# Performance work log

Hardware: AMD Instinct MI355X
Metric: run time of the kernel (lower is better)

## Reference

```python
import jax, jax.numpy as jnp
import numpy as np

M, N = 1024, 4096


def setup_inputs() -> dict:
    key = jax.random.key(0)
    k1, k2, k3 = jax.random.split(key, 3)
    scores = jax.random.normal(k1, (M, N), dtype=jnp.float32)
    continuing_ag = jax.random.randint(k2, (M,), 0, 2).astype(jnp.int32)
    joint_action_prev = jax.random.randint(k3, (M,), 0, N).astype(jnp.int32)
    return {"scores": scores, "continuing_ag": continuing_ag,
            "joint_action_prev": joint_action_prev}


def _assign(policy, continuing_ag, joint_action_prev):
    """Sequential greedy bipartite assignment (train=False / argmax path)."""
    m, n = policy.shape
    cont = continuing_ag.astype(bool)
    # Pre-assign continuing agents and zero their rows and chosen columns.
    out0 = jnp.where(cont, joint_action_prev, jnp.full((m,), -1, jnp.int32))
    col_hit = (jnp.zeros((n,), jnp.float32)
               .at[joint_action_prev].add(continuing_ag.astype(jnp.float32))) > 0
    pol0 = policy * (~cont)[:, None].astype(policy.dtype) * (~col_hit)[None, :].astype(policy.dtype)
    rows = jnp.arange(m)
    cols = jnp.arange(n)

    def step(carry, i):
        pol, act = carry
        flat = pol.reshape(-1)
        idx = jnp.argmax(flat)
        # skip if this agent is continuing, or all entries already zeroed
        do = (~cont[i]) & jnp.any(flat > 0)
        a = idx // n
        t = (idx % n).astype(act.dtype)
        act = act.at[a].set(jnp.where(do, t, act[a]))
        keep = ~((rows == a)[:, None] | (cols == (idx % n))[None, :])
        pol = jnp.where(do, pol * keep.astype(pol.dtype), pol)
        return (pol, act), None

    (_, act), _ = jax.lax.scan(step, (pol0, out0), jnp.arange(m))
    return act


def reference(scores, continuing_ag, joint_action_prev):
    # get_policy: softmax over the flattened M*N score matrix
    policy = jax.nn.softmax(scores.reshape(-1)).reshape(scores.shape)
    actions = _assign(policy, continuing_ag, joint_action_prev)
    return actions, policy
```

## Files before the change

### kernel.cpp

```cpp
#include <hip/hip_runtime.h>
#include <cstdint>
#include <cstddef>

#define MROWS 1024
#define NCOLS 4096
#define TOPK 16

typedef unsigned long long u64;
typedef unsigned int u32;

__device__ inline u32 fkey(u32 b) { return (b & 0x80000000u) ? ~b : (b | 0x80000000u); }

__device__ inline int key_col(u64 k) { return (NCOLS - 1) - (int)(k & 0xFFFull); }
__device__ inline int key_row(u64 k) { return (MROWS - 1) - (int)((k >> 12) & 0x3FFull); }

#define WAVE_FENCE() __asm__ volatile("s_waitcnt lgkmcnt(0)" ::: "memory")

__device__ inline float wave_sum_f(float v) {
    #pragma unroll
    for (int off = 32; off >= 1; off >>= 1)
        v += __shfl_xor(v, off, 64);
    return v;
}
__device__ inline u64 wave_max_u64(u64 v) {
    #pragma unroll
    for (int off = 32; off >= 1; off >>= 1) {
        u64 o = __shfl_xor(v, off, 64);
        v = o > v ? o : v;
    }
    return v;
}
__device__ inline u64 umax64(u64 a, u64 b) { return a > b ? a : b; }

#define CED(x, y) do { u64 _mx = (x) > (y) ? (x) : (y); \
                       u64 _mn = (x) > (y) ? (y) : (x); (x) = _mx; (y) = _mn; } while (0)
#define CEA(x, y) CED(y, x)

#define BMERGE16D \
    CED(a0,a8); CED(a1,a9); CED(a2,a10); CED(a3,a11); CED(a4,a12); CED(a5,a13); CED(a6,a14); CED(a7,a15); \
    CED(a0,a4); CED(a1,a5); CED(a2,a6);  CED(a3,a7);  CED(a8,a12); CED(a9,a13); CED(a10,a14); CED(a11,a15); \
    CED(a0,a2); CED(a1,a3); CED(a4,a6);  CED(a5,a7);  CED(a8,a10); CED(a9,a11); CED(a12,a14); CED(a13,a15); \
    CED(a0,a1); CED(a2,a3); CED(a4,a5);  CED(a6,a7);  CED(a8,a9);  CED(a10,a11); CED(a12,a13); CED(a14,a15);

#define SORT16D \
    CED(a0,a1); CEA(a2,a3); CED(a4,a5); CEA(a6,a7); CED(a8,a9); CEA(a10,a11); CED(a12,a13); CEA(a14,a15); \
    CED(a0,a2); CED(a1,a3); CEA(a4,a6); CEA(a5,a7); CED(a8,a10); CED(a9,a11); CEA(a12,a14); CEA(a13,a15); \
    CED(a0,a1); CED(a2,a3); CEA(a4,a5); CEA(a6,a7); CED(a8,a9); CED(a10,a11); CEA(a12,a13); CEA(a14,a15); \
    CED(a0,a4); CED(a1,a5); CED(a2,a6); CED(a3,a7); CEA(a8,a12); CEA(a9,a13); CEA(a10,a14); CEA(a11,a15); \
    CED(a0,a2); CED(a1,a3); CED(a4,a6); CED(a5,a7); CEA(a8,a10); CEA(a9,a11); CEA(a12,a14); CEA(a13,a15); \
    CED(a0,a1); CED(a2,a3); CED(a4,a5); CED(a6,a7); CEA(a8,a9); CEA(a10,a11); CEA(a12,a13); CEA(a14,a15); \
    BMERGE16D

#define HALFCLEAN \
    a0 = umax64(a0,b15); a1 = umax64(a1,b14); a2 = umax64(a2,b13); a3 = umax64(a3,b12); \
    a4 = umax64(a4,b11); a5 = umax64(a5,b10); a6 = umax64(a6,b9);  a7 = umax64(a7,b8);  \
    a8 = umax64(a8,b7);  a9 = umax64(a9,b6);  a10 = umax64(a10,b5); a11 = umax64(a11,b4); \
    a12 = umax64(a12,b3); a13 = umax64(a13,b2); a14 = umax64(a14,b1); a15 = umax64(a15,b0);

#define LDS_STORE(idx) \
    lists[0][idx]=a0; lists[1][idx]=a1; lists[2][idx]=a2; lists[3][idx]=a3; \
    lists[4][idx]=a4; lists[5][idx]=a5; lists[6][idx]=a6; lists[7][idx]=a7; \
    lists[8][idx]=a8; lists[9][idx]=a9; lists[10][idx]=a10; lists[11][idx]=a11; \
    lists[12][idx]=a12; lists[13][idx]=a13; lists[14][idx]=a14; lists[15][idx]=a15;

#define LDS_LOADB(idx) \
    b0=lists[0][idx]; b1=lists[1][idx]; b2=lists[2][idx]; b3=lists[3][idx]; \
    b4=lists[4][idx]; b5=lists[5][idx]; b6=lists[6][idx]; b7=lists[7][idx]; \
    b8=lists[8][idx]; b9=lists[9][idx]; b10=lists[10][idx]; b11=lists[11][idx]; \
    b12=lists[12][idx]; b13=lists[13][idx]; b14=lists[14][idx]; b15=lists[15][idx];

#define MERGE_LEVEL(idx) LDS_LOADB(idx); HALFCLEAN; BMERGE16D;

__global__ __launch_bounds__(256, 2) void k_prep(const float* __restrict__ s,
                                                 float* __restrict__ rowsum,
                                                 u64* __restrict__ outkeys) {
    __shared__ u64 lists[16][256];
    __shared__ float fred[4];
    int r = blockIdx.x, t = threadIdx.x;
    int wid = t >> 6, lane = t & 63;

    const float4* s4 = (const float4*)(s + (size_t)r * NCOLS);
    u64 rowpart = (u64)(MROWS - 1 - r) << 12;
    u64 a0,a1,a2,a3,a4,a5,a6,a7,a8,a9,a10,a11,a12,a13,a14,a15;
    u64 b0,b1,b2,b3,b4,b5,b6,b7,b8,b9,b10,b11,b12,b13,b14,b15;
    float acc;
    {
        float4 v0 = s4[t], v1 = s4[t + 256], v2 = s4[t + 512], v3 = s4[t + 768];
        acc  = __expf(v0.x) + __expf(v0.y) + __expf(v0.z) + __expf(v0.w);
        acc += __expf(v1.x) + __expf(v1.y) + __expf(v1.z) + __expf(v1.w);
        acc += __expf(v2.x) + __expf(v2.y) + __expf(v2.z) + __expf(v2.w);
        acc += __expf(v3.x) + __expf(v3.y) + __expf(v3.z) + __expf(v3.w);
        int c0 = 4 * t, c1 = 4 * (t + 256), c2 = 4 * (t + 512), c3 = 4 * (t + 768);
        a0  = ((u64)fkey(__float_as_uint(v0.x)) << 22) | rowpart | (u64)(NCOLS - 1 - (c0 + 0));
        a1  = ((u64)fkey(__float_as_uint(v0.y)) << 22) | rowpart | (u64)(NCOLS - 1 - (c0 + 1));
        a2  = ((u64)fkey(__float_as_uint(v0.z)) << 22) | rowpart | (u64)(NCOLS - 1 - (c0 + 2));
        a3  = ((u64)fkey(__float_as_uint(v0.w)) << 22) | rowpart | (u64)(NCOLS - 1 - (c0 + 3));
        a4  = ((u64)fkey(__float_as_uint(v1.x)) << 22) | rowpart | (u64)(NCOLS - 1 - (c1 + 0));
        a5  = ((u64)fkey(__float_as_uint(v1.y)) << 22) | rowpart | (u64)(NCOLS - 1 - (c1 + 1));
        a6  = ((u64)fkey(__float_as_uint(v1.z)) << 22) | rowpart | (u64)(NCOLS - 1 - (c1 + 2));
        a7  = ((u64)fkey(__float_as_uint(v1.w)) << 22) | rowpart | (u64)(NCOLS - 1 - (c1 + 3));
        a8  = ((u64)fkey(__float_as_uint(v2.x)) << 22) | rowpart | (u64)(NCOLS - 1 - (c2 + 0));
        a9  = ((u64)fkey(__float_as_uint(v2.y)) << 22) | rowpart | (u64)(NCOLS - 1 - (c2 + 1));
        a10 = ((u64)fkey(__float_as_uint(v2.z)) << 22) | rowpart | (u64)(NCOLS - 1 - (c2 + 2));
        a11 = ((u64)fkey(__float_as_uint(v2.w)) << 22) | rowpart | (u64)(NCOLS - 1 - (c2 + 3));
        a12 = ((u64)fkey(__float_as_uint(v3.x)) << 22) | rowpart | (u64)(NCOLS - 1 - (c3 + 0));
        a13 = ((u64)fkey(__float_as_uint(v3.y)) << 22) | rowpart | (u64)(NCOLS - 1 - (c3 + 1));
        a14 = ((u64)fkey(__float_as_uint(v3.z)) << 22) | rowpart | (u64)(NCOLS - 1 - (c3 + 2));
        a15 = ((u64)fkey(__float_as_uint(v3.w)) << 22) | rowpart | (u64)(NCOLS - 1 - (c3 + 3));
    }

    SORT16D;

    acc = wave_sum_f(acc);
    if (lane == 0) fred[wid] = acc;

    LDS_STORE(t);
    __syncthreads();
    if (t == 0) rowsum[r] = fred[0] + fred[1] + fred[2] + fred[3];

    if (t < 128) {
        MERGE_LEVEL(t + 128);
        LDS_STORE(t);
    }
    __syncthreads();

    if (t < 64) {
        MERGE_LEVEL(t + 64);
        LDS_STORE(t);
        WAVE_FENCE();
        if (t < 32) { MERGE_LEVEL(t + 32); LDS_STORE(t); }
        WAVE_FENCE();
        if (t < 16) { MERGE_LEVEL(t + 16); LDS_STORE(t); }
        WAVE_FENCE();
        if (t < 8)  { MERGE_LEVEL(t + 8);  LDS_STORE(t); }
        WAVE_FENCE();
        if (t < 4)  { MERGE_LEVEL(t + 4);  LDS_STORE(t); }
        WAVE_FENCE();
        if (t < 2)  { MERGE_LEVEL(t + 2);  LDS_STORE(t); }
        WAVE_FENCE();
        if (t == 0) {
            MERGE_LEVEL(1);
            u64* ok = outkeys + (size_t)r * TOPK;
            ok[0]=a0; ok[1]=a1; ok[2]=a2; ok[3]=a3; ok[4]=a4; ok[5]=a5; ok[6]=a6; ok[7]=a7;
            ok[8]=a8; ok[9]=a9; ok[10]=a10; ok[11]=a11; ok[12]=a12; ok[13]=a13; ok[14]=a14; ok[15]=a15;
        }
    }
}

__device__ inline u64 prune_and_best(u64* kk, const unsigned* coldone) {
    u32 cw[TOPK];
    #pragma unroll
    for (int k = 0; k < TOPK; ++k) {
        int c = key_col(kk[k]);
        cw[k] = coldone[c >> 5];
    }
    u64 best = 0ull;
    #pragma unroll
    for (int k = 0; k < TOPK; ++k) {
        int c = key_col(kk[k]);
        if ((cw[k] >> (c & 31)) & 1u) kk[k] = 0ull;
        best = umax64(best, kk[k]);
    }
    return best;
}

__global__ __launch_bounds__(512, 1) void k_policy_match(const float* __restrict__ s,
                                                         const int* __restrict__ cont,
                                                         const int* __restrict__ prev,
                                                         const float* __restrict__ rowsum,
                                                         const u64* __restrict__ keys_g,
                                                         float* __restrict__ policy,
                                                         float* __restrict__ actions) {
    __shared__ u64 colbest[NCOLS];
    __shared__ unsigned coldone[NCOLS / 32];
    __shared__ unsigned rowdone[MROWS / 32];
    __shared__ float act[MROWS];
    __shared__ float fredf[8];

    int t = threadIdx.x;
    int wid = t >> 6, lane = t & 63;

    if (blockIdx.x != 0) {
        int r = blockIdx.x - 1;
        const float4* srow4 = (const float4*)(s + (size_t)r * NCOLS);
        float4 v0 = srow4[t], v1 = srow4[t + 512];
        float sv = rowsum[t] + rowsum[t + 512];
        sv = wave_sum_f(sv);
        if (lane == 0) fredf[wid] = sv;
        __syncthreads();
        float g = 0.0f;
        #pragma unroll
        for (int i = 0; i < 8; ++i) g += fredf[i];
        float inv = 1.0f / g;
        float4* prow4 = (float4*)(policy + (size_t)r * NCOLS);
        float4 p;
        p.x = __expf(v0.x) * inv; p.y = __expf(v0.y) * inv;
        p.z = __expf(v0.z) * inv; p.w = __expf(v0.w) * inv;
        prow4[t] = p;
        p.x = __expf(v1.x) * inv; p.y = __expf(v1.y) * inv;
        p.z = __expf(v1.z) * inv; p.w = __expf(v1.w) * inv;
        prow4[t + 512] = p;
        return;
    }

    #pragma unroll
    for (int i = 0; i < 8; ++i) colbest[t + i * 512] = 0ull;
    if (t < 128) coldone[t] = 0u;
    if (t < 32) rowdone[t] = 0u;
    __syncthreads();

    int r0 = t, r1 = t + 512;
    int c0f = cont[r0], c1f = cont[r1];
    int p0 = prev[r0], p1 = prev[r1];
    act[r0] = c0f ? (float)p0 : -1.0f;
    act[r1] = c1f ? (float)p1 : -1.0f;
    if (c0f) {
        atomicOr(&rowdone[r0 >> 5], 1u << (r0 & 31));
        atomicOr(&coldone[p0 >> 5], 1u << (p0 & 31));
    }
    if (c1f) {
        atomicOr(&rowdone[r1 >> 5], 1u << (r1 & 31));
        atomicOr(&coldone[p1 >> 5], 1u << (p1 & 31));
    }
    bool act0 = (c0f == 0), act1 = (c1f == 0);

    u64 k0[TOPK], k1[TOPK];
    {
        const u64* g0 = keys_g + (size_t)r0 * TOPK;
        const u64* g1 = keys_g + (size_t)r1 * TOPK;
        #pragma unroll
        for (int k = 0; k < TOPK; ++k) { k0[k] = g0[k]; k1[k] = g1[k]; }
    }
    __syncthreads();

    for (int round = 1; round < 400; ++round) {
        u64 tag = (u64)round << 54;
        bool sub0 = false, sub1 = false;
        u64 best0 = 0ull, best1 = 0ull;
        if (act0) {
            best0 = prune_and_best(k0, coldone);
            if (best0 == 0ull) act0 = false;
            else {
                sub0 = true;
                #pragma unroll
                for (int k = 0; k < TOPK; ++k)
                    if (k0[k] != 0ull)
                        atomicMax((u64*)&colbest[key_col(k0[k])], tag | k0[k]);
            }
        }
        if (act1) {
            best1 = prune_and_best(k1, coldone);
            if (best1 == 0ull) act1 = false;
            else {
                sub1 = true;
                #pragma unroll
                for (int k = 0; k < TOPK; ++k)
                    if (k1[k] != 0ull)
                        atomicMax((u64*)&colbest[key_col(k1[k])], tag | k1[k]);
            }
        }
        __syncthreads();
        u64 cb0 = sub0 ? colbest[key_col(best0)] : 0ull;
        u64 cb1 = sub1 ? colbest[key_col(best1)] : 0ull;
        if (sub0 && cb0 == (tag | best0)) {
            int c = key_col(best0);
            unsigned old = atomicOr(&coldone[c >> 5], 1u << (c & 31));
            if (!(old & (1u << (c & 31)))) {
                act[r0] = (float)c;
                atomicOr(&rowdone[r0 >> 5], 1u << (r0 & 31));
                act0 = false;
            }
        }
        if (sub1 && cb1 == (tag | best1)) {
            int c = key_col(best1);
            unsigned old = atomicOr(&coldone[c >> 5], 1u << (c & 31));
            if (!(old & (1u << (c & 31)))) {
                act[r1] = (float)c;
                atomicOr(&rowdone[r1 >> 5], 1u << (r1 & 31));
                act1 = false;
            }
        }
        int left = __syncthreads_count((act0 || act1) ? 1 : 0);
        if (left == 0) break;
    }
    __syncthreads();

    if (t < 64) {
        unsigned miss = (t < 32) ? ~rowdone[t] : 0u;
        if (__ballot(miss != 0u) != 0ull) {
            for (int guard = 0; guard < 1200; ++guard) {
                u64 best = 0ull;
                for (int rr = 0; rr < MROWS; ++rr) {
                    if ((rowdone[rr >> 5] >> (rr & 31)) & 1u) continue;
                    const float* srow = s + (size_t)rr * NCOLS;
                    u64 rp = (u64)(MROWS - 1 - rr) << 12;
                    for (int c = t; c < NCOLS; c += 64) {
                        if ((coldone[c >> 5] >> (c & 31)) & 1u) continue;
                        u64 kk = ((u64)fkey(__float_as_uint(srow[c])) << 22) | rp |
                                 (u64)(NCOLS - 1 - c);
                        best = umax64(best, kk);
                    }
                }
                best = wave_max_u64(best);
                if (best == 0ull) break;
                if (t == 0) {
                    int row = key_row(best), col = key_col(best);
                    rowdone[row >> 5] |= 1u << (row & 31);
                    coldone[col >> 5] |= 1u << (col & 31);
                    act[row] = (float)col;
                }
                WAVE_FENCE();
            }
        }
    }
    __syncthreads();
    actions[t] = act[t];
    actions[t + 512] = act[t + 512];
}

extern "C" void kernel_launch(void* const* d_in, const int* in_sizes, int n_in,
                              void* d_out, int out_size, void* d_ws, size_t ws_size,
                              hipStream_t stream) {
    (void)in_sizes; (void)n_in; (void)out_size; (void)ws_size;
    const float* scores = (const float*)d_in[0];
    const int* cont = (const int*)d_in[1];
    const int* prev = (const int*)d_in[2];
    float* out = (float*)d_out;
    float* actions = out;
    float* policy = out + MROWS;

    char* ws = (char*)d_ws;
    float* rowsum = (float*)(ws + 0);
    u64* keys16 = (u64*)(ws + 8192);

    k_prep<<<MROWS, 256, 0, stream>>>(scores, rowsum, keys16);
    k_policy_match<<<MROWS + 1, 512, 0, stream>>>(scores, cont, prev, rowsum,
                                                  keys16, policy, actions);
}
```

Before: 102.0 us.

## Move per-row top-16 extraction into main kernel with spin-wait ready counter

Splits the prep kernel so it computes only row exp-sums. The per-row top-16 key sort moves into the policy blocks of the main kernel, each of which signals a global ready counter. Block 0, the matcher, spin-waits on that counter before starting the greedy assignment. This shortens the first kernel and overlaps key extraction with policy writing. In exchange it adds a memset launch and relies on block 0 being co-resident with the producing blocks, which risks a deadlock if scheduling order is unfavorable.

```diff
diff --git a/kernel.cpp b/kernel.cpp
--- a/kernel.cpp
+++ b/kernel.cpp
@@ -35,6 +35,13 @@
 #define CED(x, y) do { u64 _mx = (x) > (y) ? (x) : (y); \
                        u64 _mn = (x) > (y) ? (y) : (x); (x) = _mx; (y) = _mn; } while (0)
 #define CEA(x, y) CED(y, x)
+
+#define SORT8D \
+    CED(a0,a1); CEA(a2,a3); CED(a0,a2); CED(a1,a3); CED(a0,a1); CED(a2,a3); \
+    CEA(a4,a5); CED(a6,a7); CEA(a4,a6); CEA(a5,a7); CEA(a4,a5); CEA(a6,a7); \
+    CED(a0,a4); CED(a1,a5); CED(a2,a6); CED(a3,a7); \
+    CED(a0,a2); CED(a1,a3); CED(a4,a6); CED(a5,a7); \
+    CED(a0,a1); CED(a2,a3); CED(a4,a5); CED(a6,a7);
 
 #define BMERGE16D \
     CED(a0,a8); CED(a1,a9); CED(a2,a10); CED(a3,a11); CED(a4,a12); CED(a5,a13); CED(a6,a14); CED(a7,a15); \
@@ -42,112 +49,44 @@
     CED(a0,a2); CED(a1,a3); CED(a4,a6);  CED(a5,a7);  CED(a8,a10); CED(a9,a11); CED(a12,a14); CED(a13,a15); \
     CED(a0,a1); CED(a2,a3); CED(a4,a5);  CED(a6,a7);  CED(a8,a9);  CED(a10,a11); CED(a12,a13); CED(a14,a15);
 
-#define SORT16D \
-    CED(a0,a1); CEA(a2,a3); CED(a4,a5); CEA(a6,a7); CED(a8,a9); CEA(a10,a11); CED(a12,a13); CEA(a14,a15); \
-    CED(a0,a2); CED(a1,a3); CEA(a4,a6); CEA(a5,a7); CED(a8,a10); CED(a9,a11); CEA(a12,a14); CEA(a13,a15); \
-    CED(a0,a1); CED(a2,a3); CEA(a4,a5); CEA(a6,a7); CED(a8,a9); CED(a10,a11); CEA(a12,a13); CEA(a14,a15); \
-    CED(a0,a4); CED(a1,a5); CED(a2,a6); CED(a3,a7); CEA(a8,a12); CEA(a9,a13); CEA(a10,a14); CEA(a11,a15); \
-    CED(a0,a2); CED(a1,a3); CED(a4,a6); CED(a5,a7); CEA(a8,a10); CEA(a9,a11); CEA(a12,a14); CEA(a13,a15); \
-    CED(a0,a1); CED(a2,a3); CED(a4,a5); CED(a6,a7); CEA(a8,a9); CEA(a10,a11); CEA(a12,a13); CEA(a14,a15); \
-    BMERGE16D
-
 #define HALFCLEAN \
     a0 = umax64(a0,b15); a1 = umax64(a1,b14); a2 = umax64(a2,b13); a3 = umax64(a3,b12); \
     a4 = umax64(a4,b11); a5 = umax64(a5,b10); a6 = umax64(a6,b9);  a7 = umax64(a7,b8);  \
     a8 = umax64(a8,b7);  a9 = umax64(a9,b6);  a10 = umax64(a10,b5); a11 = umax64(a11,b4); \
     a12 = umax64(a12,b3); a13 = umax64(a13,b2); a14 = umax64(a14,b1); a15 = umax64(a15,b0);
 
-#define LDS_STORE(idx) \
-    lists[0][idx]=a0; lists[1][idx]=a1; lists[2][idx]=a2; lists[3][idx]=a3; \
-    lists[4][idx]=a4; lists[5][idx]=a5; lists[6][idx]=a6; lists[7][idx]=a7; \
-    lists[8][idx]=a8; lists[9][idx]=a9; lists[10][idx]=a10; lists[11][idx]=a11; \
-    lists[12][idx]=a12; lists[13][idx]=a13; lists[14][idx]=a14; lists[15][idx]=a15;
-
-#define LDS_LOADB(idx) \
-    b0=lists[0][idx]; b1=lists[1][idx]; b2=lists[2][idx]; b3=lists[3][idx]; \
-    b4=lists[4][idx]; b5=lists[5][idx]; b6=lists[6][idx]; b7=lists[7][idx]; \
-    b8=lists[8][idx]; b9=lists[9][idx]; b10=lists[10][idx]; b11=lists[11][idx]; \
-    b12=lists[12][idx]; b13=lists[13][idx]; b14=lists[14][idx]; b15=lists[15][idx];
-
-#define MERGE_LEVEL(idx) LDS_LOADB(idx); HALFCLEAN; BMERGE16D;
-
-__global__ __launch_bounds__(256, 2) void k_prep(const float* __restrict__ s,
-                                                 float* __restrict__ rowsum,
-                                                 u64* __restrict__ outkeys) {
-    __shared__ u64 lists[16][256];
+#define ST16(idx) \
+    buf16[0*256+(idx)]=a0; buf16[1*256+(idx)]=a1; buf16[2*256+(idx)]=a2; buf16[3*256+(idx)]=a3; \
+    buf16[4*256+(idx)]=a4; buf16[5*256+(idx)]=a5; buf16[6*256+(idx)]=a6; buf16[7*256+(idx)]=a7; \
+    buf16[8*256+(idx)]=a8; buf16[9*256+(idx)]=a9; buf16[10*256+(idx)]=a10; buf16[11*256+(idx)]=a11; \
+    buf16[12*256+(idx)]=a12; buf16[13*256+(idx)]=a13; buf16[14*256+(idx)]=a14; buf16[15*256+(idx)]=a15;
+
+#define LD16B(idx) \
+    b0=buf16[0*256+(idx)]; b1=buf16[1*256+(idx)]; b2=buf16[2*256+(idx)]; b3=buf16[3*256+(idx)]; \
+    b4=buf16[4*256+(idx)]; b5=buf16[5*256+(idx)]; b6=buf16[6*256+(idx)]; b7=buf16[7*256+(idx)]; \
+    b8=buf16[8*256+(idx)]; b9=buf16[9*256+(idx)]; b10=buf16[10*256+(idx)]; b11=buf16[11*256+(idx)]; \
+    b12=buf16[12*256+(idx)]; b13=buf16[13*256+(idx)]; b14=buf16[14*256+(idx)]; b15=buf16[15*256+(idx)];
+
+#define MERGE16(idx) LD16B(idx); HALFCLEAN; BMERGE16D;
+
+__global__ __launch_bounds__(256) void k_rowsum(const float* __restrict__ s,
+                                                float* __restrict__ rowsum) {
     __shared__ float fred[4];
     int r = blockIdx.x, t = threadIdx.x;
-    int wid = t >> 6, lane = t & 63;
-
     const float4* s4 = (const float4*)(s + (size_t)r * NCOLS);
-    u64 rowpart = (u64)(MROWS - 1 - r) << 12;
-    u64 a0,a1,a2,a3,a4,a5,a6,a7,a8,a9,a10,a11,a12,a13,a14,a15;
-    u64 b0,b1,b2,b3,b4,b5,b6,b7,b8,b9,b10,b11,b12,b13,b14,b15;
+    float4 v0 = s4[t], v1 = s4[t + 256], v2 = s4[t + 512], v3 = s4[t + 768];
     float acc;
-    {
-        float4 v0 = s4[t], v1 = s4[t + 256], v2 = s4[t + 512], v3 = s4[t + 768];
-        acc  = __expf(v0.x) + __expf(v0.y) + __expf(v0.z) + __expf(v0.w);
-        acc += __expf(v1.x) + __expf(v1.y) + __expf(v1.z) + __expf(v1.w);
-        acc += __expf(v2.x) + __expf(v2.y) + __expf(v2.z) + __expf(v2.w);
-        acc += __expf(v3.x) + __expf(v3.y) + __expf(v3.z) + __expf(v3.w);
-        int c0 = 4 * t, c1 = 4 * (t + 256), c2 = 4 * (t + 512), c3 = 4 * (t + 768);
-        a0  = ((u64)fkey(__float_as_uint(v0.x)) << 22) | rowpart | (u64)(NCOLS - 1 - (c0 + 0));
-        a1  = ((u64)fkey(__float_as_uint(v0.y)) << 22) | rowpart | (u64)(NCOLS - 1 - (c0 + 1));
-        a2  = ((u64)fkey(__float_as_uint(v0.z)) << 22) | rowpart | (u64)(NCOLS - 1 - (c0 + 2));
-        a3  = ((u64)fkey(__float_as_uint(v0.w)) << 22) | rowpart | (u64)(NCOLS - 1 - (c0 + 3));
-        a4  = ((u64)fkey(__float_as_uint(v1.x)) << 22) | rowpart | (u64)(NCOLS - 1 - (c1 + 0));
-        a5  = ((u64)fkey(__float_as_uint(v1.y)) << 22) | rowpart | (u64)(NCOLS - 1 - (c1 + 1));
-        a6  = ((u64)fkey(__float_as_uint(v1.z)) << 22) | rowpart | (u64)(NCOLS - 1 - (c1 + 2));
-        a7  = ((u64)fkey(__float_as_uint(v1.w)) << 22) | rowpart | (u64)(NCOLS - 1 - (c1 + 3));
-        a8  = ((u64)fkey(__float_as_uint(v2.x)) << 22) | rowpart | (u64)(NCOLS - 1 - (c2 + 0));
-        a9  = ((u64)fkey(__float_as_uint(v2.y)) << 22) | rowpart | (u64)(NCOLS - 1 - (c2 + 1));
-        a10 = ((u64)fkey(__float_as_uint(v2.z)) << 22) | rowpart | (u64)(NCOLS - 1 - (c2 + 2));
-        a11 = ((u64)fkey(__float_as_uint(v2.w)) << 22) | rowpart | (u64)(NCOLS - 1 - (c2 + 3));
-        a12 = ((u64)fkey(__float_as_uint(v3.x)) << 22) | rowpart | (u64)(NCOLS - 1 - (c3 + 0));
-        a13 = ((u64)fkey(__float_as_uint(v3.y)) << 22) | rowpart | (u64)(NCOLS - 1 - (c3 + 1));
-        a14 = ((u64)fkey(__float_as_uint(v3.z)) << 22) | rowpart | (u64)(NCOLS - 1 - (c3 + 2));
-        a15 = ((u64)fkey(__float_as_uint(v3.w)) << 22) | rowpart | (u64)(NCOLS - 1 - (c3 + 3));
-    }
-
-    SORT16D;
-
+    acc  = __expf(v0.x) + __expf(v0.y) + __expf(v0.z) + __expf(v0.w);
+    acc += __expf(v1.x) + __expf(v1.y) + __expf(v1.z) + __expf(v1.w);
+    acc += __expf(v2.x) + __expf(v2.y) + __expf(v2.z) + __expf(v2.w);
+    acc += __expf(v3.x) + __expf(v3.y) + __expf(v3.z) + __expf(v3.w);
     acc = wave_sum_f(acc);
-    if (lane == 0) fred[wid] = acc;
-
-    LDS_STORE(t);
+    if ((t & 63) == 0) fred[t >> 6] = acc;
     __syncthreads();
     if (t == 0) rowsum[r] = fred[0] + fred[1] + fred[2] + fred[3];
-
-    if (t < 128) {
-        MERGE_LEVEL(t + 128);
-        LDS_STORE(t);
-    }
-    __syncthreads();
-
-    if (t < 64) {
-        MERGE_LEVEL(t + 64);
-        LDS_STORE(t);
-        WAVE_FENCE();
-        if (t < 32) { MERGE_LEVEL(t + 32); LDS_STORE(t); }
-        WAVE_FENCE();
-        if (t < 16) { MERGE_LEVEL(t + 16); LDS_STORE(t); }
-        WAVE_FENCE();
-        if (t < 8)  { MERGE_LEVEL(t + 8);  LDS_STORE(t); }
-        WAVE_FENCE();
-        if (t < 4)  { MERGE_LEVEL(t + 4);  LDS_STORE(t); }
-        WAVE_FENCE();
-        if (t < 2)  { MERGE_LEVEL(t + 2);  LDS_STORE(t); }
-        WAVE_FENCE();
-        if (t == 0) {
-            MERGE_LEVEL(1);
-            u64* ok = outkeys + (size_t)r * TOPK;
-            ok[0]=a0; ok[1]=a1; ok[2]=a2; ok[3]=a3; ok[4]=a4; ok[5]=a5; ok[6]=a6; ok[7]=a7;
-            ok[8]=a8; ok[9]=a9; ok[10]=a10; ok[11]=a11; ok[12]=a12; ok[13]=a13; ok[14]=a14; ok[15]=a15;
-        }
-    }
-}
-
-__device__ inline u64 prune_and_best(u64* kk, const unsigned* coldone) {
+}
+
+__device__ inline u64 prune_and_best(u64* kk, const u32* coldone) {
     u32 cw[TOPK];
     #pragma unroll
     for (int k = 0; k < TOPK; ++k) {
@@ -164,29 +103,73 @@
     return best;
 }
 
-__global__ __launch_bounds__(512, 1) void k_policy_match(const float* __restrict__ s,
-                                                         const int* __restrict__ cont,
-                                                         const int* __restrict__ prev,
-                                                         const float* __restrict__ rowsum,
-                                                         const u64* __restrict__ keys_g,
-                                                         float* __restrict__ policy,
-                                                         float* __restrict__ actions) {
-    __shared__ u64 colbest[NCOLS];
-    __shared__ unsigned coldone[NCOLS / 32];
-    __shared__ unsigned rowdone[MROWS / 32];
-    __shared__ float act[MROWS];
-    __shared__ float fredf[8];
-
+__global__ __launch_bounds__(512, 2) void k_main(const float* __restrict__ s,
+                                                 const int* __restrict__ cont,
+                                                 const int* __restrict__ prev,
+                                                 const float* __restrict__ rowsum,
+                                                 u32* __restrict__ ready,
+                                                 u64* __restrict__ keys_g,
+                                                 float* __restrict__ policy,
+                                                 float* __restrict__ actions) {
+    __shared__ __align__(16) char smem[65536];
     int t = threadIdx.x;
-    int wid = t >> 6, lane = t & 63;
 
     if (blockIdx.x != 0) {
+        u64* buf8  = (u64*)smem;
+        u64* buf16 = (u64*)(smem + 32768);
         int r = blockIdx.x - 1;
-        const float4* srow4 = (const float4*)(s + (size_t)r * NCOLS);
-        float4 v0 = srow4[t], v1 = srow4[t + 512];
+        const float4* s4 = (const float4*)(s + (size_t)r * NCOLS);
+        float4 v0 = s4[t], v1 = s4[t + 512];
+        u64 rowpart = (u64)(MROWS - 1 - r) << 12;
+        u64 a0,a1,a2,a3,a4,a5,a6,a7,a8,a9,a10,a11,a12,a13,a14,a15;
+        u64 b0,b1,b2,b3,b4,b5,b6,b7,b8,b9,b10,b11,b12,b13,b14,b15;
+        {
+            int c0 = 4 * t, c1 = 4 * (t + 512);
+            a0 = ((u64)fkey(__float_as_uint(v0.x)) << 22) | rowpart | (u64)(NCOLS - 1 - (c0 + 0));
+            a1 = ((u64)fkey(__float_as_uint(v0.y)) << 22) | rowpart | (u64)(NCOLS - 1 - (c0 + 1));
+            a2 = ((u64)fkey(__float_as_uint(v0.z)) << 22) | rowpart | (u64)(NCOLS - 1 - (c0 + 2));
+            a3 = ((u64)fkey(__float_as_uint(v0.w)) << 22) | rowpart | (u64)(NCOLS - 1 - (c0 + 3));
+            a4 = ((u64)fkey(__float_as_uint(v1.x)) << 22) | rowpart | (u64)(NCOLS - 1 - (c1 + 0));
+            a5 = ((u64)fkey(__float_as_uint(v1.y)) << 22) | rowpart | (u64)(NCOLS - 1 - (c1 + 1));
+            a6 = ((u64)fkey(__float_as_uint(v1.z)) << 22) | rowpart | (u64)(NCOLS - 1 - (c1 + 2));
+            a7 = ((u64)fkey(__float_as_uint(v1.w)) << 22) | rowpart | (u64)(NCOLS - 1 - (c1 + 3));
+        }
+        SORT8D;
+        buf8[0*512+t]=a0; buf8[1*512+t]=a1; buf8[2*512+t]=a2; buf8[3*512+t]=a3;
+        buf8[4*512+t]=a4; buf8[5*512+t]=a5; buf8[6*512+t]=a6; buf8[7*512+t]=a7;
+        __syncthreads();
+        if (t < 256) {
+            int u = t + 256;
+            a8  = buf8[7*512+u]; a9  = buf8[6*512+u]; a10 = buf8[5*512+u]; a11 = buf8[4*512+u];
+            a12 = buf8[3*512+u]; a13 = buf8[2*512+u]; a14 = buf8[1*512+u]; a15 = buf8[0*512+u];
+            BMERGE16D;
+            ST16(t);
+        }
+        __syncthreads();
+        if (t < 128) { MERGE16(t + 128); ST16(t); }
+        __syncthreads();
+        if (t < 64) {
+            MERGE16(t + 64); ST16(t);
+            WAVE_FENCE();
+            if (t < 32) { MERGE16(t + 32); ST16(t); } WAVE_FENCE();
+            if (t < 16) { MERGE16(t + 16); ST16(t); } WAVE_FENCE();
+            if (t < 8)  { MERGE16(t + 8);  ST16(t); } WAVE_FENCE();
+            if (t < 4)  { MERGE16(t + 4);  ST16(t); } WAVE_FENCE();
+            if (t < 2)  { MERGE16(t + 2);  ST16(t); } WAVE_FENCE();
+            if (t == 0) {
+                MERGE16(1);
+                u64* ok = keys_g + (size_t)r * TOPK;
+                ok[0]=a0; ok[1]=a1; ok[2]=a2; ok[3]=a3; ok[4]=a4; ok[5]=a5; ok[6]=a6; ok[7]=a7;
+                ok[8]=a8; ok[9]=a9; ok[10]=a10; ok[11]=a11; ok[12]=a12; ok[13]=a13; ok[14]=a14; ok[15]=a15;
+                __threadfence();
+                __hip_atomic_fetch_add(ready, 1u, __ATOMIC_RELEASE, __HIP_MEMORY_SCOPE_AGENT);
+            }
+        }
+        __syncthreads();
+        float* fredf = (float*)smem;
         float sv = rowsum[t] + rowsum[t + 512];
         sv = wave_sum_f(sv);
-        if (lane == 0) fredf[wid] = sv;
+        if ((t & 63) == 0) fredf[t >> 6] = sv;
         __syncthreads();
         float g = 0.0f;
         #pragma unroll
@@ -203,6 +186,20 @@
         return;
     }
 
+    u64* colbest = (u64*)smem;
+    u32* coldone = (u32*)(smem + 32768);
+    u32* rowdone = (u32*)(smem + 33280);
+    float* act   = (float*)(smem + 33408);
+
+    if (t == 0) {
+        for (long i = 0; i < 2000000000L; ++i) {
+            if (__hip_atomic_load(ready, __ATOMIC_ACQUIRE, __HIP_MEMORY_SCOPE_AGENT) >= MROWS)
+                break;
+            __builtin_amdgcn_s_sleep(1);
+        }
+    }
+    __syncthreads();
+
     #pragma unroll
     for (int i = 0; i < 8; ++i) colbest[t + i * 512] = 0ull;
     if (t < 128) coldone[t] = 0u;
@@ -264,7 +261,7 @@
         u64 cb1 = sub1 ? colbest[key_col(best1)] : 0ull;
         if (sub0 && cb0 == (tag | best0)) {
             int c = key_col(best0);
-            unsigned old = atomicOr(&coldone[c >> 5], 1u << (c & 31));
+            u32 old = atomicOr(&coldone[c >> 5], 1u << (c & 31));
             if (!(old & (1u << (c & 31)))) {
                 act[r0] = (float)c;
                 atomicOr(&rowdone[r0 >> 5], 1u << (r0 & 31));
@@ -273,7 +270,7 @@
         }
         if (sub1 && cb1 == (tag | best1)) {
             int c = key_col(best1);
-            unsigned old = atomicOr(&coldone[c >> 5], 1u << (c & 31));
+            u32 old = atomicOr(&coldone[c >> 5], 1u << (c & 31));
             if (!(old & (1u << (c & 31)))) {
                 act[r1] = (float)c;
                 atomicOr(&rowdone[r1 >> 5], 1u << (r1 & 31));
@@ -286,7 +283,7 @@
     __syncthreads();
 
     if (t < 64) {
-        unsigned miss = (t < 32) ? ~rowdone[t] : 0u;
+        u32 miss = (t < 32) ? ~rowdone[t] : 0u;
         if (__ballot(miss != 0u) != 0ull) {
             for (int guard = 0; guard < 1200; ++guard) {
                 u64 best = 0ull;
@@ -331,9 +328,11 @@
 
     char* ws = (char*)d_ws;
     float* rowsum = (float*)(ws + 0);
+    u32* ready = (u32*)(ws + 4096);
     u64* keys16 = (u64*)(ws + 8192);
 
-    k_prep<<<MROWS, 256, 0, stream>>>(scores, rowsum, keys16);
-    k_policy_match<<<MROWS + 1, 512, 0, stream>>>(scores, cont, prev, rowsum,
-                                                  keys16, policy, actions);
-}
+    hipMemsetAsync(ready, 0, 4, stream);
+    k_rowsum<<<MROWS, 256, 0, stream>>>(scores, rowsum);
+    k_main<<<MROWS + 1, 512, 0, stream>>>(scores, cont, prev, rowsum, ready,
+                                          keys16, policy, actions);
+}
```

Result: slower. 160.4 us (+57.2%).
